# Kernel tuning notes

Measured on AMD Instinct MI355X. Metric: run time of the kernel, lower is better.

Reference implementation:

```python
import jax, jax.numpy as jnp
import numpy as np

D_MODEL = 1024
NUM_HEADS = 16
D_K = D_MODEL // NUM_HEADS
B, N = 2, 2048


def setup_inputs() -> dict:
    key = jax.random.key(0)
    ks = jax.random.split(key, 11)
    s = 1.0 / np.sqrt(D_MODEL)
    inp = {
        "query": jax.random.normal(ks[0], (B, N, D_MODEL), jnp.float32),
        "key": jax.random.normal(ks[1], (B, N, D_MODEL), jnp.float32),
        "value": jax.random.normal(ks[2], (B, N, D_MODEL), jnp.float32),
        "w_q": jax.random.normal(ks[3], (D_MODEL, D_MODEL), jnp.float32) * s,
        "b_q": jax.random.normal(ks[4], (D_MODEL,), jnp.float32) * s,
        "w_k": jax.random.normal(ks[5], (D_MODEL, D_MODEL), jnp.float32) * s,
        "b_k": jax.random.normal(ks[6], (D_MODEL,), jnp.float32) * s,
        "w_v": jax.random.normal(ks[7], (D_MODEL, D_MODEL), jnp.float32) * s,
        "b_v": jax.random.normal(ks[8], (D_MODEL,), jnp.float32) * s,
        "w_o": jax.random.normal(ks[9], (D_MODEL, D_MODEL), jnp.float32) * s,
        "b_o": jax.random.normal(ks[10], (D_MODEL,), jnp.float32) * s,
    }
    return inp


def reference(query, key, value, w_q, b_q, w_k, b_k, w_v, b_v, w_o, b_o):
    Bq, Nq, _ = query.shape
    # projections (torch Linear: x @ W.T + b)
    Q = (query @ w_q.T + b_q).reshape(Bq, Nq, NUM_HEADS, D_K).transpose(0, 2, 1, 3)
    K = (key @ w_k.T + b_k).reshape(Bq, -1, NUM_HEADS, D_K).transpose(0, 2, 1, 3)
    V = (value @ w_v.T + b_v).reshape(Bq, -1, NUM_HEADS, D_K).transpose(0, 2, 1, 3)
    scores = jnp.einsum("bhqd,bhkd->bhqk", Q, K) / np.sqrt(D_K).astype(np.float32)
    attn = jax.nn.softmax(scores, axis=-1)  # dropout p=0.0 -> identity
    ctx = jnp.einsum("bhqk,bhkd->bhqd", attn, V)
    ctx = ctx.transpose(0, 2, 1, 3).reshape(Bq, Nq, D_MODEL)
    return ctx @ w_o.T + b_o
```

## Files before the change

kernel.cpp:

```cpp
#include <hip/hip_runtime.h>
#include <math.h>

#define D_MODEL 1024
#define NUM_HEADS 16
#define DK 64
#define BATCH 2
#define NSEQ 2048
#define MROWS (BATCH * NSEQ)

typedef __attribute__((ext_vector_type(8))) short bf16x8;
typedef __attribute__((ext_vector_type(4))) short s16x4;
typedef __attribute__((ext_vector_type(4))) float f32x4;
typedef unsigned short u16;

static __device__ __forceinline__ u16 f2bf_rne(float x) {
    union { float f; unsigned u; } v; v.f = x;
    unsigned r = v.u + 0x7fffu + ((v.u >> 16) & 1u);
    return (u16)(r >> 16);
}
static __device__ __forceinline__ void split_bf16(float x, u16& hi, u16& lo) {
    union { float f; unsigned u; } v; v.f = x;
    unsigned hb = v.u & 0xffff0000u;
    hi = (u16)(hb >> 16);
    union { unsigned u; float f; } hv; hv.u = hb;
    lo = f2bf_rne(x - hv.f);
}

#define AS1 __attribute__((address_space(1)))
#define AS3 __attribute__((address_space(3)))
static __device__ __forceinline__ void gl_lds16(const void* g, void* l) {
    __builtin_amdgcn_global_load_lds((AS1 void*)(uintptr_t)g, (AS3 void*)l, 16, 0, 0);
}

struct SplitN { const float* src[4]; u16* h[4]; u16* l[4]; };
__global__ __launch_bounds__(256)
void split_multi(SplitN args, int n8)
{
    const int w = blockIdx.y;
    const int i = blockIdx.x * 256 + threadIdx.x;
    if (i >= n8) return;
    const float* src = args.src[w];
    float4 a = ((const float4*)src)[2 * i];
    float4 b = ((const float4*)src)[2 * i + 1];
    float x[8] = {a.x, a.y, a.z, a.w, b.x, b.y, b.z, b.w};
    u16 hh[8], ll[8];
#pragma unroll
    for (int j = 0; j < 8; ++j) split_bf16(x[j], hh[j], ll[j]);
    *(uint4*)(args.h[w] + 8 * (size_t)i) = *(uint4*)hh;
    *(uint4*)(args.l[w] + 8 * (size_t)i) = *(uint4*)ll;
}

struct GemmDesc {
    const u16 *Ah, *Al, *Wh, *Wl;
    const float* bias;
    float* outF;
    u16 *outH, *outL;
    float scale;
    int mode;
};
struct GemmBatch { GemmDesc d[3]; };

template<int MT>
__global__ __launch_bounds__(256)
void gemm_mfma_v2(GemmBatch batch, int M, int N, int K)
{
    constexpr int BM = MT * 32;
    __shared__ u16 SM[(2 * BM + 2 * 128) * 32];
    u16* As_h = SM;
    u16* As_l = As_h + BM * 32;
    u16* Ws_h = As_l + BM * 32;
    u16* Ws_l = Ws_h + 128 * 32;

    const GemmDesc d = batch.d[blockIdx.z];
    const int tid  = threadIdx.x;
    const int wv   = tid >> 6, lane = tid & 63;
    const int quad = lane >> 4, lcol = lane & 15;
    const int bm = blockIdx.y * BM, bn = blockIdx.x * 128;
    const int wm = (wv >> 1) * (MT * 16), wn = (wv & 1) * 64;
    const int srow = lane >> 2;
    const int g4o  = (((lane & 3) ^ (srow & 3)) << 3);
    const int xk   = (lcol & 3);

    f32x4 acc[MT][4];
#pragma unroll
    for (int i = 0; i < MT; ++i)
#pragma unroll
        for (int j = 0; j < 4; ++j) acc[i][j] = (f32x4){0.f, 0.f, 0.f, 0.f};

    constexpr int AIPW = BM / 64;

    for (int k0 = 0; k0 < K; k0 += 32) {
        __syncthreads();
#pragma unroll
        for (int c = 0; c < AIPW; ++c) {
            const int rb = (wv * AIPW + c) * 16;
            gl_lds16(d.Ah + (size_t)(bm + rb + srow) * K + k0 + g4o, As_h + rb * 32);
            gl_lds16(d.Al + (size_t)(bm + rb + srow) * K + k0 + g4o, As_l + rb * 32);
        }
#pragma unroll
        for (int c = 0; c < 2; ++c) {
            const int rb = (wv * 2 + c) * 16;
            gl_lds16(d.Wh + (size_t)(bn + rb + srow) * K + k0 + g4o, Ws_h + rb * 32);
            gl_lds16(d.Wl + (size_t)(bn + rb + srow) * K + k0 + g4o, Ws_l + rb * 32);
        }
        __syncthreads();

        bf16x8 bh[4], bl[4];
#pragma unroll
        for (int j = 0; j < 4; ++j) {
            const int off = (wn + (j << 4) + lcol) * 32 + ((quad ^ xk) << 3);
            bh[j] = *(const bf16x8*)(Ws_h + off);
            bl[j] = *(const bf16x8*)(Ws_l + off);
        }
#pragma unroll
        for (int i = 0; i < MT; ++i) {
            const int off = (wm + (i << 4) + lcol) * 32 + ((quad ^ xk) << 3);
            bf16x8 ah = *(const bf16x8*)(As_h + off);
            bf16x8 al = *(const bf16x8*)(As_l + off);
#pragma unroll
            for (int j = 0; j < 4; ++j) {
                acc[i][j] = __builtin_amdgcn_mfma_f32_16x16x32_bf16(ah, bh[j], acc[i][j], 0, 0, 0);
                acc[i][j] = __builtin_amdgcn_mfma_f32_16x16x32_bf16(al, bh[j], acc[i][j], 0, 0, 0);
                acc[i][j] = __builtin_amdgcn_mfma_f32_16x16x32_bf16(ah, bl[j], acc[i][j], 0, 0, 0);
            }
        }
    }

    if constexpr (MT == 4) {
        if (batch.d[blockIdx.z].mode == 2) {
            u16* T = SM;
#pragma unroll
            for (int p = 0; p < 2; ++p) {
                __syncthreads();
                if ((wv & 1) == p) {
#pragma unroll
                    for (int j = 0; j < 4; ++j) {
                        const int cl = (j << 4) + lcol;
                        const float bj = d.bias[bn + wn + (j << 4) + lcol];
#pragma unroll
                        for (int i = 0; i < 4; ++i) {
                            u16 pk[4];
#pragma unroll
                            for (int r = 0; r < 4; ++r)
                                pk[r] = f2bf_rne(acc[i][j][r] + bj);
                            *(ushort4*)(T + cl * 136 + wm + (i << 4) + quad * 4) = *(ushort4*)pk;
                        }
                    }
                }
                __syncthreads();
                const int dd = tid >> 2, nt = tid & 3;
                u16* dst = d.outH
                    + ((size_t)((bm >> 11) * NUM_HEADS + (bn >> 6) + p) * DK + dd) * NSEQ
                    + (bm & (NSEQ - 1)) + nt * 32;
                const u16* srcT = T + dd * 136 + nt * 32;
#pragma unroll
                for (int k = 0; k < 4; ++k)
                    ((uint4*)dst)[k] = *(const uint4*)(srcT + 8 * k);
            }
            return;
        }
    }

#pragma unroll
    for (int j = 0; j < 4; ++j) {
        const int col = bn + wn + (j << 4) + lcol;
        const float bj = d.bias[col];
#pragma unroll
        for (int i = 0; i < MT; ++i) {
#pragma unroll
            for (int r = 0; r < 4; ++r) {
                const int row = bm + wm + (i << 4) + quad * 4 + r;
                const float v = (acc[i][j][r] + bj) * d.scale;
                const size_t o = (size_t)row * N + col;
                if (d.mode == 0) {
                    d.outF[o] = v;
                } else {
                    u16 hi, lo;
                    split_bf16(v, hi, lo);
                    d.outH[o] = hi;
                    d.outL[o] = lo;
                }
            }
        }
    }
}

__global__ __launch_bounds__(256)
void flash_attn(const u16* __restrict__ Qh_g, const u16* __restrict__ Ql_g,
                const u16* __restrict__ Kh_g, const u16* __restrict__ Kl_g,
                const u16* __restrict__ Vt_g,
                u16* __restrict__ Ch_g, u16* __restrict__ Cl_g)
{
    __shared__ __align__(16) u16 Ks_h[64 * 64], Ks_l[64 * 64], Vs[64 * 64];

    const int tid  = threadIdx.x;
    const int wv   = tid >> 6;
    const int lane = tid & 63;
    const int quad = lane >> 4;
    const int lcol = lane & 15;
    const int q0   = blockIdx.x << 7;
    const int h    = blockIdx.y;
    const int b    = blockIdx.z;
    const size_t hbase  = (size_t)b * NSEQ * D_MODEL + (size_t)h * DK;
    const size_t vtbase = (size_t)(b * NUM_HEADS + h) * DK * NSEQ;

    bf16x8 bQh[2][2], bQl[2][2];
#pragma unroll
    for (int s = 0; s < 2; ++s) {
        const u16* qh = Qh_g + hbase + (size_t)(q0 + wv * 32 + s * 16 + lcol) * D_MODEL;
        const u16* ql = Ql_g + hbase + (size_t)(q0 + wv * 32 + s * 16 + lcol) * D_MODEL;
#pragma unroll
        for (int c = 0; c < 2; ++c) {
            bQh[s][c] = *(const bf16x8*)(qh + c * 32 + quad * 8);
            bQl[s][c] = *(const bf16x8*)(ql + c * 32 + quad * 8);
        }
    }

    f32x4 Oacc[2][4];
#pragma unroll
    for (int s = 0; s < 2; ++s)
#pragma unroll
        for (int t = 0; t < 4; ++t) Oacc[s][t] = (f32x4){0.f, 0.f, 0.f, 0.f};
    float mrow[2] = {-INFINITY, -INFINITY};
    float lrow[2] = {0.f, 0.f};

    const int srow8 = lane >> 3;
    const int g8o   = (((lane & 7) ^ srow8) << 3);
    const int xk    = (lcol & 7);

    for (int kt = 0; kt < NSEQ / 64; ++kt) {
        const int k0 = kt << 6;
        __syncthreads();
#pragma unroll
        for (int c = 0; c < 2; ++c) {
            const int rb = wv * 16 + c * 8;
            gl_lds16(Kh_g + hbase + (size_t)(k0 + rb + srow8) * D_MODEL + g8o, Ks_h + rb * 64);
            gl_lds16(Kl_g + hbase + (size_t)(k0 + rb + srow8) * D_MODEL + g8o, Ks_l + rb * 64);
            gl_lds16(Vt_g + vtbase + (size_t)(rb + srow8) * NSEQ + k0 + g8o, Vs + rb * 64);
        }
        __syncthreads();

        f32x4 S[2][4];
#pragma unroll
        for (int t = 0; t < 4; ++t) {
            const u16* krh = Ks_h + ((t << 4) + lcol) * 64;
            const u16* krl = Ks_l + ((t << 4) + lcol) * 64;
            const int s0 = ((quad ^ xk) << 3);
            const int s1 = (((4 + quad) ^ xk) << 3);
            bf16x8 aKh0 = *(const bf16x8*)(krh + s0);
            bf16x8 aKh1 = *(const bf16x8*)(krh + s1);
            bf16x8 aKl0 = *(const bf16x8*)(krl + s0);
            bf16x8 aKl1 = *(const bf16x8*)(krl + s1);
#pragma unroll
            for (int s = 0; s < 2; ++s) {
                f32x4 a = (f32x4){0.f, 0.f, 0.f, 0.f};
                a = __builtin_amdgcn_mfma_f32_16x16x32_bf16(aKh0, bQh[s][0], a, 0, 0, 0);
                a = __builtin_amdgcn_mfma_f32_16x16x32_bf16(aKh1, bQh[s][1], a, 0, 0, 0);
                a = __builtin_amdgcn_mfma_f32_16x16x32_bf16(aKl0, bQh[s][0], a, 0, 0, 0);
                a = __builtin_amdgcn_mfma_f32_16x16x32_bf16(aKl1, bQh[s][1], a, 0, 0, 0);
                a = __builtin_amdgcn_mfma_f32_16x16x32_bf16(aKh0, bQl[s][0], a, 0, 0, 0);
                a = __builtin_amdgcn_mfma_f32_16x16x32_bf16(aKh1, bQl[s][1], a, 0, 0, 0);
                S[s][t] = a;
            }
        }

        bf16x8 pb[2][2];
#pragma unroll
        for (int s = 0; s < 2; ++s) {
            float m16 = -INFINITY;
#pragma unroll
            for (int t = 0; t < 4; ++t)
#pragma unroll
                for (int r = 0; r < 4; ++r) m16 = fmaxf(m16, S[s][t][r]);
            m16 = fmaxf(m16, __shfl_xor(m16, 16, 64));
            m16 = fmaxf(m16, __shfl_xor(m16, 32, 64));
            const float mn = fmaxf(mrow[s], m16);
            const float alpha = __expf(mrow[s] - mn);
            mrow[s] = mn;

            float p[4][4];
            float psum = 0.f;
#pragma unroll
            for (int t = 0; t < 4; ++t)
#pragma unroll
                for (int r = 0; r < 4; ++r) {
                    const float pv = __expf(S[s][t][r] - mn);
                    p[t][r] = pv;
                    psum += pv;
                }
            psum += __shfl_xor(psum, 16, 64);
            psum += __shfl_xor(psum, 32, 64);
            lrow[s] = alpha * lrow[s] + psum;

#pragma unroll
            for (int c = 0; c < 2; ++c) {
                bf16x8 v;
#pragma unroll
                for (int r = 0; r < 4; ++r) {
                    v[r]     = (short)f2bf_rne(p[2 * c][r]);
                    v[4 + r] = (short)f2bf_rne(p[2 * c + 1][r]);
                }
                pb[s][c] = v;
            }
#pragma unroll
            for (int t = 0; t < 4; ++t)
#pragma unroll
                for (int r = 0; r < 4; ++r) Oacc[s][t][r] *= alpha;
        }

#pragma unroll
        for (int dt = 0; dt < 4; ++dt) {
            const u16* vr = Vs + ((dt << 4) + lcol) * 64;
#pragma unroll
            for (int c = 0; c < 2; ++c) {
                const int s0 = (((c * 4 + (quad >> 1)) ^ xk) << 3) + ((quad & 1) << 2);
                s16x4 alo = *(const s16x4*)(vr + s0);
                s16x4 ahi = *(const s16x4*)(vr + (s0 ^ 16));
                bf16x8 aV;
#pragma unroll
                for (int r = 0; r < 4; ++r) { aV[r] = alo[r]; aV[4 + r] = ahi[r]; }
#pragma unroll
                for (int s = 0; s < 2; ++s)
                    Oacc[s][dt] = __builtin_amdgcn_mfma_f32_16x16x32_bf16(aV, pb[s][c], Oacc[s][dt], 0, 0, 0);
            }
        }
    }

#pragma unroll
    for (int s = 0; s < 2; ++s) {
        const float inv = 1.f / lrow[s];
        const size_t base = hbase + (size_t)(q0 + wv * 32 + s * 16 + lcol) * D_MODEL;
#pragma unroll
        for (int dt = 0; dt < 4; ++dt) {
            u16 hv[4], lv[4];
#pragma unroll
            for (int r = 0; r < 4; ++r)
                split_bf16(Oacc[s][dt][r] * inv, hv[r], lv[r]);
            const size_t o = base + (dt << 4) + quad * 4;
            *(ushort4*)(Ch_g + o) = *(ushort4*)hv;
            *(ushort4*)(Cl_g + o) = *(ushort4*)lv;
        }
    }
}

extern "C" void kernel_launch(void* const* d_in, const int* in_sizes, int n_in,
                              void* d_out, int out_size, void* d_ws, size_t ws_size,
                              hipStream_t stream)
{
    const float* query = (const float*)d_in[0];
    const float* key_i = (const float*)d_in[1];
    const float* value = (const float*)d_in[2];
    const float* w_q   = (const float*)d_in[3];
    const float* b_q   = (const float*)d_in[4];
    const float* w_k   = (const float*)d_in[5];
    const float* b_k   = (const float*)d_in[6];
    const float* w_v   = (const float*)d_in[7];
    const float* b_v   = (const float*)d_in[8];
    const float* w_o   = (const float*)d_in[9];
    const float* b_o   = (const float*)d_in[10];
    float* out = (float*)d_out;

    const size_t WE = (size_t)D_MODEL * D_MODEL;
    const size_t AE = (size_t)MROWS * D_MODEL;

    u16* p = (u16*)d_ws;
    u16* Wqh = p;            u16* Wql = Wqh + WE;
    u16* Wkh = Wql + WE;     u16* Wkl = Wkh + WE;
    u16* Wvh = Wkl + WE;     u16* Wvl = Wvh + WE;
    u16* Woh = Wvl + WE;     u16* Wol = Woh + WE;
    u16* base = Wol + WE;

    SplitN ws4;
    ws4.src[0] = w_q; ws4.h[0] = Wqh; ws4.l[0] = Wql;
    ws4.src[1] = w_k; ws4.h[1] = Wkh; ws4.l[1] = Wkl;
    ws4.src[2] = w_v; ws4.h[2] = Wvh; ws4.l[2] = Wvl;
    ws4.src[3] = w_o; ws4.h[3] = Woh; ws4.l[3] = Wol;
    split_multi<<<dim3((unsigned)(WE / 8 / 256), 4), 256, 0, stream>>>(ws4, (int)(WE / 8));

    const float qscale = 0.125f;
    dim3 fgrid(NSEQ / 128, NUM_HEADS, BATCH);
    dim3 qkvgrid(D_MODEL / 128, MROWS / 128, 3);
    dim3 outgrid(D_MODEL / 128, MROWS / 64, 1);
    dim3 qkvgrid1(D_MODEL / 128, MROWS / 128, 1);
    const int an8 = (int)(AE / 8);

    const size_t fused_bytes = 2 * (8 * WE + 11 * AE);
    if (ws_size >= fused_bytes) {
        u16* INqh = base;          u16* INql = INqh + AE;
        u16* INkh = INql + AE;     u16* INkl = INkh + AE;
        u16* INvh = INkl + AE;     u16* INvl = INvh + AE;
        u16* Qph  = INvl + AE;     u16* Qpl  = Qph + AE;
        u16* Kph  = Qpl + AE;      u16* Kpl  = Kph + AE;
        u16* VT   = Kpl + AE;
        u16* Ch   = INqh;          u16* Cl   = INql;

        SplitN as3;
        as3.src[0] = query; as3.h[0] = INqh; as3.l[0] = INql;
        as3.src[1] = key_i; as3.h[1] = INkh; as3.l[1] = INkl;
        as3.src[2] = value; as3.h[2] = INvh; as3.l[2] = INvl;
        as3.src[3] = query; as3.h[3] = INqh; as3.l[3] = INql;
        split_multi<<<dim3((unsigned)(AE / 8 / 256), 3), 256, 0, stream>>>(as3, an8);

        GemmBatch gb;
        gb.d[0] = {INqh, INql, Wqh, Wql, b_q, nullptr, Qph, Qpl, qscale, 1};
        gb.d[1] = {INkh, INkl, Wkh, Wkl, b_k, nullptr, Kph, Kpl, 1.0f,   1};
        gb.d[2] = {INvh, INvl, Wvh, Wvl, b_v, nullptr, VT,  nullptr, 1.0f, 2};
        gemm_mfma_v2<4><<<qkvgrid, 256, 0, stream>>>(gb, MROWS, D_MODEL, D_MODEL);

        flash_attn<<<fgrid, 256, 0, stream>>>(Qph, Qpl, Kph, Kpl, VT, Ch, Cl);

        GemmBatch go;
        go.d[0] = {Ch, Cl, Woh, Wol, b_o, out, nullptr, nullptr, 1.0f, 0};
        gemm_mfma_v2<2><<<outgrid, 256, 0, stream>>>(go, MROWS, D_MODEL, D_MODEL);
    } else {
        u16* INh = base;           u16* INl = INh + AE;
        u16* Qph = INl + AE;       u16* Qpl = Qph + AE;
        u16* Kph = Qpl + AE;       u16* Kpl = Kph + AE;
        u16* VT  = Kpl + AE;
        u16* Ch  = INh;            u16* Cl  = INl;

        SplitN s1;
        s1.src[0] = query; s1.h[0] = INh; s1.l[0] = INl;
        s1.src[1] = s1.src[2] = s1.src[3] = query;
        s1.h[1] = s1.h[2] = s1.h[3] = INh; s1.l[1] = s1.l[2] = s1.l[3] = INl;

        GemmBatch g;
        s1.src[0] = query;
        split_multi<<<dim3((unsigned)(AE / 8 / 256), 1), 256, 0, stream>>>(s1, an8);
        g.d[0] = {INh, INl, Wqh, Wql, b_q, nullptr, Qph, Qpl, qscale, 1};
        gemm_mfma_v2<4><<<qkvgrid1, 256, 0, stream>>>(g, MROWS, D_MODEL, D_MODEL);

        s1.src[0] = key_i;
        split_multi<<<dim3((unsigned)(AE / 8 / 256), 1), 256, 0, stream>>>(s1, an8);
        g.d[0] = {INh, INl, Wkh, Wkl, b_k, nullptr, Kph, Kpl, 1.0f, 1};
        gemm_mfma_v2<4><<<qkvgrid1, 256, 0, stream>>>(g, MROWS, D_MODEL, D_MODEL);

        s1.src[0] = value;
        split_multi<<<dim3((unsigned)(AE / 8 / 256), 1), 256, 0, stream>>>(s1, an8);
        g.d[0] = {INh, INl, Wvh, Wvl, b_v, nullptr, VT, nullptr, 1.0f, 2};
        gemm_mfma_v2<4><<<qkvgrid1, 256, 0, stream>>>(g, MROWS, D_MODEL, D_MODEL);

        flash_attn<<<fgrid, 256, 0, stream>>>(Qph, Qpl, Kph, Kpl, VT, Ch, Cl);

        g.d[0] = {Ch, Cl, Woh, Wol, b_o, out, nullptr, nullptr, 1.0f, 0};
        gemm_mfma_v2<2><<<outgrid, 256, 0, stream>>>(g, MROWS, D_MODEL, D_MODEL);
    }
}
```

Measured before the change: 365.6 us.

## Fuse activation bf16 splitting into GEMM loads and drop direct-to-LDS copies

The GEMM now reads fp32 activations directly, splits them into hi/lo bf16 in registers and stores them to LDS, with register prefetch of the next K tile. This removes the separate activation split kernel and its round trip through memory. Flash attention switches from global_load_lds to padded LDS with register staging and writes an fp32 context that the output GEMM splits itself. The grid is swapped to M-major, and the fallback path for a small workspace is removed. In exchange, the split arithmetic moves into the GEMM inner loop and more registers are used, while the async LDS loads are lost.

```diff
diff --git a/kernel.cpp b/kernel.cpp
--- a/kernel.cpp
+++ b/kernel.cpp
@@ -24,12 +24,6 @@
     hi = (u16)(hb >> 16);
     union { unsigned u; float f; } hv; hv.u = hb;
     lo = f2bf_rne(x - hv.f);
-}
-
-#define AS1 __attribute__((address_space(1)))
-#define AS3 __attribute__((address_space(3)))
-static __device__ __forceinline__ void gl_lds16(const void* g, void* l) {
-    __builtin_amdgcn_global_load_lds((AS1 void*)(uintptr_t)g, (AS3 void*)l, 16, 0, 0);
 }
 
 struct SplitN { const float* src[4]; u16* h[4]; u16* l[4]; };
@@ -51,7 +45,8 @@
 }
 
 struct GemmDesc {
-    const u16 *Ah, *Al, *Wh, *Wl;
+    const float* Af;
+    const u16 *Wh, *Wl;
     const float* bias;
     float* outF;
     u16 *outH, *outL;
@@ -62,7 +57,7 @@
 
 template<int MT>
 __global__ __launch_bounds__(256)
-void gemm_mfma_v2(GemmBatch batch, int M, int N, int K)
+void gemm_v3(GemmBatch batch, int M, int N, int K)
 {
     constexpr int BM = MT * 32;
     __shared__ u16 SM[(2 * BM + 2 * 128) * 32];
@@ -75,11 +70,70 @@
     const int tid  = threadIdx.x;
     const int wv   = tid >> 6, lane = tid & 63;
     const int quad = lane >> 4, lcol = lane & 15;
-    const int bm = blockIdx.y * BM, bn = blockIdx.x * 128;
+    const int bm = blockIdx.x * BM, bn = blockIdx.y * 128;
     const int wm = (wv >> 1) * (MT * 16), wn = (wv & 1) * 64;
-    const int srow = lane >> 2;
-    const int g4o  = (((lane & 3) ^ (srow & 3)) << 3);
-    const int xk   = (lcol & 3);
+
+    int asr, ash;
+    if constexpr (MT == 4) { asr = tid >> 1; ash = tid & 1; }
+    else                   { asr = tid >> 2; ash = tid & 3; }
+    const int mA = (asr & 3) ^ ((asr >> 2) & 3);
+    const int wsr = tid >> 1, wsh = tid & 1;
+    const int mW = (wsr & 3) ^ ((wsr >> 2) & 3);
+
+    const float* Ap  = d.Af + (size_t)(bm + asr) * K;
+    const u16*   Whp = d.Wh + (size_t)(bn + wsr) * K;
+    const u16*   Wlp = d.Wl + (size_t)(bn + wsr) * K;
+
+    float4 Ar[MT];
+    uint4  Wrh[2], Wrl[2];
+
+    auto loadT = [&](int k0) {
+        if constexpr (MT == 4) {
+            const float4* ap = (const float4*)(Ap + k0 + ash * 16);
+#pragma unroll
+            for (int i = 0; i < 4; ++i) Ar[i] = ap[i];
+        } else {
+            const float4* ap = (const float4*)(Ap + k0 + ash * 8);
+            Ar[0] = ap[0]; Ar[1] = ap[1];
+        }
+        const uint4* wph = (const uint4*)(Whp + k0 + wsh * 16);
+        const uint4* wpl = (const uint4*)(Wlp + k0 + wsh * 16);
+        Wrh[0] = wph[0]; Wrh[1] = wph[1];
+        Wrl[0] = wpl[0]; Wrl[1] = wpl[1];
+    };
+
+    auto storeT = [&]() {
+        const float* af = (const float*)Ar;
+        if constexpr (MT == 4) {
+            u16 h[16], l[16];
+#pragma unroll
+            for (int t = 0; t < 16; ++t) split_bf16(af[t], h[t], l[t]);
+            u16* dh = As_h + asr * 32 + ((ash ^ (mA >> 1)) << 4);
+            u16* dl = As_l + asr * 32 + ((ash ^ (mA >> 1)) << 4);
+            const int o0 = (mA & 1) * 8, o1 = o0 ^ 8;
+            *(uint4*)(dh + o0) = *(uint4*)(h + 0);
+            *(uint4*)(dh + o1) = *(uint4*)(h + 8);
+            *(uint4*)(dl + o0) = *(uint4*)(l + 0);
+            *(uint4*)(dl + o1) = *(uint4*)(l + 8);
+        } else {
+            u16 h[8], l[8];
+#pragma unroll
+            for (int t = 0; t < 8; ++t) split_bf16(af[t], h[t], l[t]);
+            const int s = 2 * ((ash >> 1) ^ (mA >> 1)) + ((ash & 1) ^ (mA & 1));
+            *(uint4*)(As_h + asr * 32 + s * 8) = *(uint4*)h;
+            *(uint4*)(As_l + asr * 32 + s * 8) = *(uint4*)l;
+        }
+        u16* dh = Ws_h + wsr * 32 + ((wsh ^ (mW >> 1)) << 4);
+        u16* dl = Ws_l + wsr * 32 + ((wsh ^ (mW >> 1)) << 4);
+        const int o0 = (mW & 1) * 8, o1 = o0 ^ 8;
+        *(uint4*)(dh + o0) = Wrh[0];
+        *(uint4*)(dh + o1) = Wrh[1];
+        *(uint4*)(dl + o0) = Wrl[0];
+        *(uint4*)(dl + o1) = Wrl[1];
+    };
+
+    const int mm = (lcol & 3) ^ ((lcol >> 2) & 3);
+    const int sF = (2 * ((quad >> 1) ^ (mm >> 1)) + ((quad & 1) ^ (mm & 1))) * 8;
 
     f32x4 acc[MT][4];
 #pragma unroll
@@ -87,34 +141,24 @@
 #pragma unroll
         for (int j = 0; j < 4; ++j) acc[i][j] = (f32x4){0.f, 0.f, 0.f, 0.f};
 
-    constexpr int AIPW = BM / 64;
-
-    for (int k0 = 0; k0 < K; k0 += 32) {
+    loadT(0);
+    const int KT = K / 32;
+    for (int kt = 0; kt < KT; ++kt) {
+        if (kt) __syncthreads();
+        storeT();
         __syncthreads();
-#pragma unroll
-        for (int c = 0; c < AIPW; ++c) {
-            const int rb = (wv * AIPW + c) * 16;
-            gl_lds16(d.Ah + (size_t)(bm + rb + srow) * K + k0 + g4o, As_h + rb * 32);
-            gl_lds16(d.Al + (size_t)(bm + rb + srow) * K + k0 + g4o, As_l + rb * 32);
-        }
-#pragma unroll
-        for (int c = 0; c < 2; ++c) {
-            const int rb = (wv * 2 + c) * 16;
-            gl_lds16(d.Wh + (size_t)(bn + rb + srow) * K + k0 + g4o, Ws_h + rb * 32);
-            gl_lds16(d.Wl + (size_t)(bn + rb + srow) * K + k0 + g4o, Ws_l + rb * 32);
-        }
-        __syncthreads();
+        if (kt + 1 < KT) loadT((kt + 1) * 32);
 
         bf16x8 bh[4], bl[4];
 #pragma unroll
         for (int j = 0; j < 4; ++j) {
-            const int off = (wn + (j << 4) + lcol) * 32 + ((quad ^ xk) << 3);
+            const int off = (wn + (j << 4) + lcol) * 32 + sF;
             bh[j] = *(const bf16x8*)(Ws_h + off);
             bl[j] = *(const bf16x8*)(Ws_l + off);
         }
 #pragma unroll
         for (int i = 0; i < MT; ++i) {
-            const int off = (wm + (i << 4) + lcol) * 32 + ((quad ^ xk) << 3);
+            const int off = (wm + (i << 4) + lcol) * 32 + sF;
             bf16x8 ah = *(const bf16x8*)(As_h + off);
             bf16x8 al = *(const bf16x8*)(As_l + off);
 #pragma unroll
@@ -189,9 +233,10 @@
 void flash_attn(const u16* __restrict__ Qh_g, const u16* __restrict__ Ql_g,
                 const u16* __restrict__ Kh_g, const u16* __restrict__ Kl_g,
                 const u16* __restrict__ Vt_g,
-                u16* __restrict__ Ch_g, u16* __restrict__ Cl_g)
+                float* __restrict__ Ctx)
 {
-    __shared__ __align__(16) u16 Ks_h[64 * 64], Ks_l[64 * 64], Vs[64 * 64];
+    __shared__ __align__(16) u16 Ks_h[64][72], Ks_l[64][72];
+    __shared__ __align__(16) u16 Vs[64][72];
 
     const int tid  = threadIdx.x;
     const int wv   = tid >> 6;
@@ -224,33 +269,32 @@
     float mrow[2] = {-INFINITY, -INFINITY};
     float lrow[2] = {0.f, 0.f};
 
-    const int srow8 = lane >> 3;
-    const int g8o   = (((lane & 7) ^ srow8) << 3);
-    const int xk    = (lcol & 7);
+    const int lr = tid >> 2;
+    const int lc = (tid & 3) << 4;
 
     for (int kt = 0; kt < NSEQ / 64; ++kt) {
         const int k0 = kt << 6;
         __syncthreads();
-#pragma unroll
-        for (int c = 0; c < 2; ++c) {
-            const int rb = wv * 16 + c * 8;
-            gl_lds16(Kh_g + hbase + (size_t)(k0 + rb + srow8) * D_MODEL + g8o, Ks_h + rb * 64);
-            gl_lds16(Kl_g + hbase + (size_t)(k0 + rb + srow8) * D_MODEL + g8o, Ks_l + rb * 64);
-            gl_lds16(Vt_g + vtbase + (size_t)(rb + srow8) * NSEQ + k0 + g8o, Vs + rb * 64);
+        {
+            const u16* skh = Kh_g + hbase + (size_t)(k0 + lr) * D_MODEL + lc;
+            const u16* skl = Kl_g + hbase + (size_t)(k0 + lr) * D_MODEL + lc;
+            const u16* sv  = Vt_g + vtbase + (size_t)lr * NSEQ + k0 + lc;
+            *(uint4*)&Ks_h[lr][lc]     = *(const uint4*)skh;
+            *(uint4*)&Ks_h[lr][lc + 8] = *(const uint4*)(skh + 8);
+            *(uint4*)&Ks_l[lr][lc]     = *(const uint4*)skl;
+            *(uint4*)&Ks_l[lr][lc + 8] = *(const uint4*)(skl + 8);
+            *(uint4*)&Vs[lr][lc]       = *(const uint4*)sv;
+            *(uint4*)&Vs[lr][lc + 8]   = *(const uint4*)(sv + 8);
         }
         __syncthreads();
 
         f32x4 S[2][4];
 #pragma unroll
         for (int t = 0; t < 4; ++t) {
-            const u16* krh = Ks_h + ((t << 4) + lcol) * 64;
-            const u16* krl = Ks_l + ((t << 4) + lcol) * 64;
-            const int s0 = ((quad ^ xk) << 3);
-            const int s1 = (((4 + quad) ^ xk) << 3);
-            bf16x8 aKh0 = *(const bf16x8*)(krh + s0);
-            bf16x8 aKh1 = *(const bf16x8*)(krh + s1);
-            bf16x8 aKl0 = *(const bf16x8*)(krl + s0);
-            bf16x8 aKl1 = *(const bf16x8*)(krl + s1);
+            bf16x8 aKh0 = *(const bf16x8*)&Ks_h[(t << 4) + lcol][quad * 8];
+            bf16x8 aKh1 = *(const bf16x8*)&Ks_h[(t << 4) + lcol][32 + quad * 8];
+            bf16x8 aKl0 = *(const bf16x8*)&Ks_l[(t << 4) + lcol][quad * 8];
+            bf16x8 aKl1 = *(const bf16x8*)&Ks_l[(t << 4) + lcol][32 + quad * 8];
 #pragma unroll
             for (int s = 0; s < 2; ++s) {
                 f32x4 a = (f32x4){0.f, 0.f, 0.f, 0.f};
@@ -310,12 +354,11 @@
 
 #pragma unroll
         for (int dt = 0; dt < 4; ++dt) {
-            const u16* vr = Vs + ((dt << 4) + lcol) * 64;
+            const u16* vr = &Vs[(dt << 4) + lcol][0];
 #pragma unroll
             for (int c = 0; c < 2; ++c) {
-                const int s0 = (((c * 4 + (quad >> 1)) ^ xk) << 3) + ((quad & 1) << 2);
-                s16x4 alo = *(const s16x4*)(vr + s0);
-                s16x4 ahi = *(const s16x4*)(vr + (s0 ^ 16));
+                s16x4 alo = *(const s16x4*)(vr + c * 32 + quad * 4);
+                s16x4 ahi = *(const s16x4*)(vr + c * 32 + 16 + quad * 4);
                 bf16x8 aV;
 #pragma unroll
                 for (int r = 0; r < 4; ++r) { aV[r] = alo[r]; aV[4 + r] = ahi[r]; }
@@ -332,13 +375,12 @@
         const size_t base = hbase + (size_t)(q0 + wv * 32 + s * 16 + lcol) * D_MODEL;
 #pragma unroll
         for (int dt = 0; dt < 4; ++dt) {
-            u16 hv[4], lv[4];
-#pragma unroll
-            for (int r = 0; r < 4; ++r)
-                split_bf16(Oacc[s][dt][r] * inv, hv[r], lv[r]);
-            const size_t o = base + (dt << 4) + quad * 4;
-            *(ushort4*)(Ch_g + o) = *(ushort4*)hv;
-            *(ushort4*)(Cl_g + o) = *(ushort4*)lv;
+            float4 v;
+            v.x = Oacc[s][dt][0] * inv;
+            v.y = Oacc[s][dt][1] * inv;
+            v.z = Oacc[s][dt][2] * inv;
+            v.w = Oacc[s][dt][3] * inv;
+            *(float4*)(Ctx + base + (dt << 4) + quad * 4) = v;
         }
     }
 }
@@ -368,7 +410,10 @@
     u16* Wkh = Wql + WE;     u16* Wkl = Wkh + WE;
     u16* Wvh = Wkl + WE;     u16* Wvl = Wvh + WE;
     u16* Woh = Wvl + WE;     u16* Wol = Woh + WE;
-    u16* base = Wol + WE;
+    u16* Qh  = Wol + WE;     u16* Ql  = Qh + AE;
+    u16* Kh  = Ql + AE;      u16* Kl  = Kh + AE;
+    u16* VT  = Kl + AE;
+    float* CTX = (float*)(VT + AE);
 
     SplitN ws4;
     ws4.src[0] = w_q; ws4.h[0] = Wqh; ws4.l[0] = Wql;
@@ -377,72 +422,15 @@
     ws4.src[3] = w_o; ws4.h[3] = Woh; ws4.l[3] = Wol;
     split_multi<<<dim3((unsigned)(WE / 8 / 256), 4), 256, 0, stream>>>(ws4, (int)(WE / 8));
 
-    const float qscale = 0.125f;
-    dim3 fgrid(NSEQ / 128, NUM_HEADS, BATCH);
-    dim3 qkvgrid(D_MODEL / 128, MROWS / 128, 3);
-    dim3 outgrid(D_MODEL / 128, MROWS / 64, 1);
-    dim3 qkvgrid1(D_MODEL / 128, MROWS / 128, 1);
-    const int an8 = (int)(AE / 8);
-
-    const size_t fused_bytes = 2 * (8 * WE + 11 * AE);
-    if (ws_size >= fused_bytes) {
-        u16* INqh = base;          u16* INql = INqh + AE;
-        u16* INkh = INql + AE;     u16* INkl = INkh + AE;
-        u16* INvh = INkl + AE;     u16* INvl = INvh + AE;
-        u16* Qph  = INvl + AE;     u16* Qpl  = Qph + AE;
-        u16* Kph  = Qpl + AE;      u16* Kpl  = Kph + AE;
-        u16* VT   = Kpl + AE;
-        u16* Ch   = INqh;          u16* Cl   = INql;
-
-        SplitN as3;
-        as3.src[0] = query; as3.h[0] = INqh; as3.l[0] = INql;
-        as3.src[1] = key_i; as3.h[1] = INkh; as3.l[1] = INkl;
-        as3.src[2] = value; as3.h[2] = INvh; as3.l[2] = INvl;
-        as3.src[3] = query; as3.h[3] = INqh; as3.l[3] = INql;
-        split_multi<<<dim3((unsigned)(AE / 8 / 256), 3), 256, 0, stream>>>(as3, an8);
-
-        GemmBatch gb;
-        gb.d[0] = {INqh, INql, Wqh, Wql, b_q, nullptr, Qph, Qpl, qscale, 1};
-        gb.d[1] = {INkh, INkl, Wkh, Wkl, b_k, nullptr, Kph, Kpl, 1.0f,   1};
-        gb.d[2] = {INvh, INvl, Wvh, Wvl, b_v, nullptr, VT,  nullptr, 1.0f, 2};
-        gemm_mfma_v2<4><<<qkvgrid, 256, 0, stream>>>(gb, MROWS, D_MODEL, D_MODEL);
-
-        flash_attn<<<fgrid, 256, 0, stream>>>(Qph, Qpl, Kph, Kpl, VT, Ch, Cl);
-
-        GemmBatch go;
-        go.d[0] = {Ch, Cl, Woh, Wol, b_o, out, nullptr, nullptr, 1.0f, 0};
-        gemm_mfma_v2<2><<<outgrid, 256, 0, stream>>>(go, MROWS, D_MODEL, D_MODEL);
-    } else {
-        u16* INh = base;           u16* INl = INh + AE;
-        u16* Qph = INl + AE;       u16* Qpl = Qph + AE;
-        u16* Kph = Qpl + AE;       u16* Kpl = Kph + AE;
-        u16* VT  = Kpl + AE;
-        u16* Ch  = INh;            u16* Cl  = INl;
-
-        SplitN s1;
-        s1.src[0] = query; s1.h[0] = INh; s1.l[0] = INl;
-        s1.src[1] = s1.src[2] = s1.src[3] = query;
-        s1.h[1] = s1.h[2] = s1.h[3] = INh; s1.l[1] = s1.l[2] = s1.l[3] = INl;
-
-        GemmBatch g;
-        s1.src[0] = query;
-        split_multi<<<dim3((unsigned)(AE / 8 / 256), 1), 256, 0, stream>>>(s1, an8);
-        g.d[0] = {INh, INl, Wqh, Wql, b_q, nullptr, Qph, Qpl, qscale, 1};
-        gemm_mfma_v2<4><<<qkvgrid1, 256, 0, stream>>>(g, MROWS, D_MODEL, D_MODEL);
-
-        s1.src[0] = key_i;
-        split_multi<<<dim3((unsigned)(AE / 8 / 256), 1), 256, 0, stream>>>(s1, an8);
-        g.d[0] = {INh, INl, Wkh, Wkl, b_k, nullptr, Kph, Kpl, 1.0f, 1};
-        gemm_mfma_v2<4><<<qkvgrid1, 256, 0, stream>>>(g, MROWS, D_MODEL, D_MODEL);
-
-        s1.src[0] = value;
-        split_multi<<<dim3((unsigned)(AE / 8 / 256), 1), 256, 0, stream>>>(s1, an8);
-        g.d[0] = {INh, INl, Wvh, Wvl, b_v, nullptr, VT, nullptr, 1.0f, 2};
-        gemm_mfma_v2<4><<<qkvgrid1, 256, 0, stream>>>(g, MROWS, D_MODEL, D_MODEL);
-
-        flash_attn<<<fgrid, 256, 0, stream>>>(Qph, Qpl, Kph, Kpl, VT, Ch, Cl);
-
-        g.d[0] = {Ch, Cl, Woh, Wol, b_o, out, nullptr, nullptr, 1.0f, 0};
-        gemm_mfma_v2<2><<<outgrid, 256, 0, stream>>>(g, MROWS, D_MODEL, D_MODEL);
-    }
-}
+    GemmBatch gb;
+    gb.d[0] = {query, Wqh, Wql, b_q, nullptr, Qh, Ql, 0.125f, 1};
+    gb.d[1] = {key_i, Wkh, Wkl, b_k, nullptr, Kh, Kl, 1.0f,   1};
+    gb.d[2] = {value, Wvh, Wvl, b_v, nullptr, VT,  nullptr, 1.0f, 2};
+    gemm_v3<4><<<dim3(MROWS / 128, D_MODEL / 128, 3), 256, 0, stream>>>(gb, MROWS, D_MODEL, D_MODEL);
+
+    flash_attn<<<dim3(NSEQ / 128, NUM_HEADS, BATCH), 256, 0, stream>>>(Qh, Ql, Kh, Kl, VT, CTX);
+
+    GemmBatch go;
+    go.d[0] = {CTX, Woh, Wol, b_o, out, nullptr, nullptr, 1.0f, 0};
+    gemm_v3<2><<<dim3(MROWS / 64, D_MODEL / 128, 1), 256, 0, stream>>>(go, MROWS, D_MODEL, D_MODEL);
+}
```

After: 456.4 us. +24.8%, slower.
